# Optimization experiments

Hardware: AMD Instinct MI355X
Metric: run time of the kernel (lower is better)

Reference implementation:

```python
import jax, jax.numpy as jnp
import numpy as np

NEG = -10000.0

def setup_inputs() -> dict:
    key = jax.random.key(0)
    ks = jax.random.split(key, 8)
    B, S, D = 16, 1024, 768
    scale = 1.0 / np.sqrt(D)
    return {
        "q": jax.random.normal(ks[0], (B, S, D), jnp.float32),
        "k": jax.random.normal(ks[1], (B, S, D), jnp.float32),
        "v": jax.random.normal(ks[2], (B, S, D), jnp.float32),
        "Wq": jax.random.normal(ks[3], (D, D), jnp.float32) * scale,
        "bq": jnp.zeros((D,), jnp.float32),
        "Wk": jax.random.normal(ks[4], (D, D), jnp.float32) * scale,
        "bk": jnp.zeros((D,), jnp.float32),
        "Wv": jax.random.normal(ks[5], (D, D), jnp.float32) * scale,
        "bv": jnp.zeros((D,), jnp.float32),
        "temperature": jnp.float32(1.0),
    }

def reference(q, k, v, Wq, bq, Wk, bk, Wv, bv, temperature):
    # Linear projections (torch Linear: x @ W.T + b; here W stored as [out,in])
    Q = jnp.einsum("bsd,ed->bse", q, Wq) + bq  # [B,S,Dq]
    K = jnp.einsum("bsd,ed->bse", k, Wk) + bk  # [B,S,Dk]
    V = jnp.einsum("bsd,ed->bse", v, Wv) + bv  # [B,S,Dv]
    scores = jnp.einsum("bqe,bke->bqk", Q, K) / temperature  # [B,S,S]
    S = scores.shape[-1]
    diag = jnp.eye(S, dtype=bool)  # diagonal self-exclusion mask
    scores = jnp.where(diag[None, :, :], NEG, scores)
    attn = jax.nn.softmax(scores, axis=-1)
    return jnp.einsum("bqk,bke->bqe", attn, V)
```

## Files before the change

kernel.cpp:

```cpp
#include <hip/hip_runtime.h>
#include <math.h>


typedef _Float16 f16x8 __attribute__((ext_vector_type(8)));
typedef _Float16 f16x4 __attribute__((ext_vector_type(4)));
typedef __attribute__((ext_vector_type(4))) float f32x4;

template<typename T>
__device__ __forceinline__ void async_copy16(T* lds, const T* g) {
    __builtin_amdgcn_global_load_lds(
        (const __attribute__((address_space(1))) unsigned int*)g,
        (__attribute__((address_space(3))) unsigned int*)lds, 16, 0, 0);
}

__device__ __forceinline__ void barrier_mem() {
    asm volatile("s_barrier" ::: "memory");
}

template<int EPI, int BIAS>
__global__ __launch_bounds__(512, 2)
void mfma_gemm256(const _Float16* __restrict__ A, const _Float16* __restrict__ B,
                  const float* __restrict__ bias, void* __restrict__ C0,
                  int K, int lda, int ldb, int ldc,
                  long long sA, long long sB, long long sC)
{
    __shared__ _Float16 smem[65536];

    const int tid = threadIdx.x;

    const int gx = gridDim.x, gy = gridDim.y;
    const int nwg = gx * gy * gridDim.z;
    const int p = blockIdx.x + gx * (blockIdx.y + gy * blockIdx.z);
    const int cpx = nwg >> 3;
    const int l = (nwg & 7) ? p : (p & 7) * cpx + (p >> 3);
    const int bx = l % gx;
    const int by = (l / gx) % gy;
    const long long bz = l / (gx * gy);
    const int m0 = by * 256, n0 = bx * 256;

    const _Float16* A0 = A + bz * sA;
    const _Float16* B0 = B + bz * sB;

    const int lane = tid & 63;
    const int wid  = tid >> 6;
    const int wm   = wid >> 2;
    const int wn   = wid & 3;
    const int fr   = lane & 15;
    const int fs   = lane >> 4;

    const int nt = K / 64;
    const int iters = nt / 2;

    auto stage_unit = [&](int dbuf, int isB, int unit, int tile) {
        if (tile >= nt) return;
        const int kt = tile * 64;
        const int lr = tid >> 3, s = tid & 7;
        const int grow = isB ? (unit * 64 + lr)
                             : (((lr >> 5) << 7) + unit * 32 + (lr & 31));
        const int gslot = s ^ (grow & 7);
        _Float16* dst = smem + dbuf * 32768 + isB * 16384 + grow * 64 + s * 8;
        const _Float16* src = (isB ? B0 : A0)
            + (size_t)((isB ? n0 : m0) + grow) * (size_t)(isB ? ldb : lda)
            + kt + gslot * 8;
        async_copy16(dst, src);
    };

    f32x4 acc[8][4] = {};
    f16x8 bf[4][2];

#define PHASE(BUF, Q, READB, STAGES, VMW) do {                                 \
    const _Float16* Ab = smem + (BUF) * 32768;                                 \
    const _Float16* Bb = Ab + 16384;                                           \
    f16x8 a0k0, a0k1, a1k0, a1k1;                                              \
    { const int r = wm * 128 + ((Q) * 2 + 0) * 16 + fr;                        \
      a0k0 = *(const f16x8*)&Ab[r * 64 + ((fs       ^ (r & 7)) * 8)];          \
      a0k1 = *(const f16x8*)&Ab[r * 64 + (((4 + fs) ^ (r & 7)) * 8)]; }        \
    { const int r = wm * 128 + ((Q) * 2 + 1) * 16 + fr;                        \
      a1k0 = *(const f16x8*)&Ab[r * 64 + ((fs       ^ (r & 7)) * 8)];          \
      a1k1 = *(const f16x8*)&Ab[r * 64 + (((4 + fs) ^ (r & 7)) * 8)]; }        \
    if (READB) {                                                               \
      _Pragma("unroll") for (int ni = 0; ni < 4; ++ni) {                       \
        const int r = wn * 64 + ni * 16 + fr;                                  \
        bf[ni][0] = *(const f16x8*)&Bb[r * 64 + ((fs       ^ (r & 7)) * 8)];   \
        bf[ni][1] = *(const f16x8*)&Bb[r * 64 + (((4 + fs) ^ (r & 7)) * 8)]; } \
    }                                                                          \
    STAGES;                                                                    \
    barrier_mem();                                                             \
    __builtin_amdgcn_s_setprio(1);                                             \
    _Pragma("unroll") for (int ni = 0; ni < 4; ++ni) {                         \
      acc[(Q)*2+0][ni] = __builtin_amdgcn_mfma_f32_16x16x32_f16(a0k0, bf[ni][0], acc[(Q)*2+0][ni], 0, 0, 0); \
      acc[(Q)*2+0][ni] = __builtin_amdgcn_mfma_f32_16x16x32_f16(a0k1, bf[ni][1], acc[(Q)*2+0][ni], 0, 0, 0); \
      acc[(Q)*2+1][ni] = __builtin_amdgcn_mfma_f32_16x16x32_f16(a1k0, bf[ni][0], acc[(Q)*2+1][ni], 0, 0, 0); \
      acc[(Q)*2+1][ni] = __builtin_amdgcn_mfma_f32_16x16x32_f16(a1k1, bf[ni][1], acc[(Q)*2+1][ni], 0, 0, 0); \
    }                                                                          \
    __builtin_amdgcn_s_setprio(0);                                             \
    VMW;                                                                       \
    barrier_mem();                                                             \
} while (0)

    stage_unit(0, 0, 0, 0); stage_unit(0, 0, 1, 0);
    stage_unit(0, 0, 2, 0); stage_unit(0, 0, 3, 0);
    stage_unit(0, 1, 0, 0); stage_unit(0, 1, 1, 0);
    stage_unit(0, 1, 2, 0); stage_unit(0, 1, 3, 0);
    stage_unit(1, 1, 0, 1); stage_unit(1, 1, 1, 1);
    stage_unit(1, 1, 2, 1); stage_unit(1, 1, 3, 1);
    stage_unit(1, 0, 0, 1); stage_unit(1, 0, 1, 1);
    asm volatile("s_waitcnt vmcnt(6)" ::: "memory");
    barrier_mem();

    for (int i = 0; i < iters; ++i) {
        const int T1 = 2 * i + 1, T2 = 2 * i + 2, T3 = 2 * i + 3;
        const bool last = (i + 1 == iters);
        PHASE(0, 0, 1, stage_unit(1, 0, 2, T1); stage_unit(1, 0, 3, T1), );
        PHASE(0, 1, 0, stage_unit(0, 1, 0, T2); stage_unit(0, 1, 1, T2), );
        PHASE(0, 2, 0, stage_unit(0, 1, 2, T2); stage_unit(0, 1, 3, T2), );
        PHASE(0, 3, 0, stage_unit(0, 0, 0, T2); stage_unit(0, 0, 1, T2),
              if (last) { asm volatile("s_waitcnt vmcnt(0)" ::: "memory"); }
              else      { asm volatile("s_waitcnt vmcnt(6)" ::: "memory"); });
        PHASE(1, 0, 1, stage_unit(0, 0, 2, T2); stage_unit(0, 0, 3, T2), );
        PHASE(1, 1, 0, stage_unit(1, 1, 0, T3); stage_unit(1, 1, 1, T3), );
        PHASE(1, 2, 0, stage_unit(1, 1, 2, T3); stage_unit(1, 1, 3, T3), );
        PHASE(1, 3, 0, stage_unit(1, 0, 0, T3); stage_unit(1, 0, 1, T3),
              asm volatile("s_waitcnt vmcnt(6)" ::: "memory"));
    }
#undef PHASE

    #pragma unroll
    for (int mi = 0; mi < 8; ++mi) {
        #pragma unroll
        for (int ni = 0; ni < 4; ++ni) {
            const int col = n0 + wn * 64 + ni * 16 + fr;
            #pragma unroll
            for (int r = 0; r < 4; ++r) {
                const int row = m0 + wm * 128 + mi * 16 + fs * 4 + r;
                float vv = acc[mi][ni][r];
                if (BIAS == 1) vv += bias[col];
                if (BIAS == 2) vv += bias[row];
                const size_t idx = (size_t)bz * sC + (size_t)row * ldc + col;
                if (EPI == 0) ((float*)C0)[idx] = vv;
                else          ((_Float16*)C0)[idx] = (_Float16)vv;
            }
        }
    }
}

template<int EPI, int BIAS>
__global__ __launch_bounds__(256, 2)
void mfma_gemm(const _Float16* __restrict__ A, const _Float16* __restrict__ B,
               const float* __restrict__ bias,
               void* __restrict__ C0,
               int K, int lda, int ldb, int ldc,
               long long sA, long long sB, long long sC)
{
    __shared__ _Float16 sAh[128 * 32];
    __shared__ _Float16 sBh[128 * 32];

    const int tid = threadIdx.x;
    const int gx = gridDim.x, gy = gridDim.y;
    const int nwg = gx * gy * gridDim.z;
    const int p = blockIdx.x + gx * (blockIdx.y + gy * blockIdx.z);
    const int cpx = nwg >> 3;
    const int l = (nwg & 7) ? p : (p & 7) * cpx + (p >> 3);
    const int bx = l % gx;
    const int by = (l / gx) % gy;
    const long long bz = l / (gx * gy);

    const int m0 = by * 128;
    const int n0 = bx * 128;

    const _Float16* A0 = A + bz * sA;
    const _Float16* B0 = B + bz * sB;

    const int lrow  = tid >> 2;
    const int lslot = tid & 3;

    const int lane = tid & 63;
    const int wv   = tid >> 6;
    const int wm   = wv >> 1, wn = wv & 1;
    const int fr   = lane & 15;
    const int fs   = lane >> 4;
    const int sw   = fs ^ (fr & 3);
    const int abase = (wm * 64 + fr) * 32 + sw * 8;
    const int bbase = (wn * 64 + fr) * 32 + sw * 8;

    f32x4 acc[4][4] = {};

    for (int kt = 0; kt < K; kt += 32) {
        #pragma unroll
        for (int it = 0; it < 2; ++it) {
            const int row = lrow + it * 64;
            const int gsl = (lslot ^ (row & 3)) << 3;
            const size_t loff = (size_t)tid * 8 + (size_t)it * 2048;
            async_copy16(&sAh[loff], A0 + (size_t)(m0 + row) * lda + kt + gsl);
            async_copy16(&sBh[loff], B0 + (size_t)(n0 + row) * ldb + kt + gsl);
        }
        __syncthreads();

        f16x8 ah[4], bh[4];
        #pragma unroll
        for (int i = 0; i < 4; ++i) {
            ah[i] = *(const f16x8*)&sAh[abase + i * 512];
            bh[i] = *(const f16x8*)&sBh[bbase + i * 512];
        }
        #pragma unroll
        for (int mi = 0; mi < 4; ++mi)
            #pragma unroll
            for (int ni = 0; ni < 4; ++ni)
                acc[mi][ni] = __builtin_amdgcn_mfma_f32_16x16x32_f16(
                    ah[mi], bh[ni], acc[mi][ni], 0, 0, 0);
        __syncthreads();
    }

    const int er = fs * 4;
    #pragma unroll
    for (int mi = 0; mi < 4; ++mi) {
        #pragma unroll
        for (int ni = 0; ni < 4; ++ni) {
            const int col = n0 + wn * 64 + ni * 16 + fr;
            #pragma unroll
            for (int r = 0; r < 4; ++r) {
                const int row = m0 + wm * 64 + mi * 16 + er + r;
                float vv = acc[mi][ni][r];
                if (BIAS == 1) vv += bias[col];
                if (BIAS == 2) vv += bias[row];
                const size_t idx = (size_t)bz * sC + (size_t)row * ldc + col;
                if (EPI == 0) ((float*)C0)[idx] = vv;
                else          ((_Float16*)C0)[idx] = (_Float16)vv;
            }
        }
    }
}

__global__ __launch_bounds__(256)
void tof16_3(const float* __restrict__ q, const float* __restrict__ k,
             const float* __restrict__ v,
             _Float16* __restrict__ qh, _Float16* __restrict__ kh,
             _Float16* __restrict__ vh)
{
    const float* src = blockIdx.z == 0 ? q : blockIdx.z == 1 ? k : v;
    _Float16* dst    = blockIdx.z == 0 ? qh : blockIdx.z == 1 ? kh : vh;
    const long long i = ((long long)blockIdx.x * 256 + threadIdx.x) * 16;
    const float4 a = *(const float4*)&src[i];
    const float4 b = *(const float4*)&src[i + 4];
    const float4 c = *(const float4*)&src[i + 8];
    const float4 d = *(const float4*)&src[i + 12];
    f16x8 o0, o1;
    o0[0] = (_Float16)a.x; o0[1] = (_Float16)a.y;
    o0[2] = (_Float16)a.z; o0[3] = (_Float16)a.w;
    o0[4] = (_Float16)b.x; o0[5] = (_Float16)b.y;
    o0[6] = (_Float16)b.z; o0[7] = (_Float16)b.w;
    o1[0] = (_Float16)c.x; o1[1] = (_Float16)c.y;
    o1[2] = (_Float16)c.z; o1[3] = (_Float16)c.w;
    o1[4] = (_Float16)d.x; o1[5] = (_Float16)d.y;
    o1[6] = (_Float16)d.z; o1[7] = (_Float16)d.w;
    *(f16x8*)&dst[i] = o0;
    *(f16x8*)&dst[i + 8] = o1;
}

__global__ __launch_bounds__(256)
void tof16_kernel(const float* __restrict__ src, _Float16* __restrict__ dst,
                  long long n)
{
    long long i = ((long long)blockIdx.x * 256 + threadIdx.x) * 8;
    const long long stride = (long long)gridDim.x * 2048;
    for (; i < n; i += stride) {
        const float4 a = *(const float4*)&src[i];
        const float4 b = *(const float4*)&src[i + 4];
        f16x8 o;
        o[0] = (_Float16)a.x; o[1] = (_Float16)a.y;
        o[2] = (_Float16)a.z; o[3] = (_Float16)a.w;
        o[4] = (_Float16)b.x; o[5] = (_Float16)b.y;
        o[6] = (_Float16)b.z; o[7] = (_Float16)b.w;
        *(f16x8*)&dst[i] = o;
    }
}

__global__ __launch_bounds__(256)
void transpose_f16(const float* __restrict__ src, _Float16* __restrict__ dst, int n)
{
    __shared__ float t[64][65];
    const int tx = threadIdx.x & 63, ty = threadIdx.x >> 6;
    const int r0 = blockIdx.y * 64, c0 = blockIdx.x * 64;
    #pragma unroll
    for (int r = 0; r < 16; ++r) {
        const int row = ty * 16 + r;
        t[row][tx] = src[(size_t)(r0 + row) * n + c0 + tx];
    }
    __syncthreads();
    #pragma unroll
    for (int r = 0; r < 16; ++r) {
        const int orow = ty * 16 + r;
        dst[(size_t)(c0 + orow) * n + r0 + tx] = (_Float16)t[tx][orow];
    }
}

__global__ __launch_bounds__(256)
void colvec_kernel(const _Float16* __restrict__ WkT, const float* __restrict__ bq,
                   float* __restrict__ colvec, int n)
{
    const int wv = threadIdx.x >> 6, lane = threadIdx.x & 63;
    const int d = blockIdx.x * 4 + wv;
    float s = 0.f;
    for (int e = lane; e < n; e += 64)
        s += (float)WkT[(size_t)d * n + e] * bq[e];
    #pragma unroll
    for (int off = 32; off; off >>= 1) s += __shfl_down(s, off, 64);
    if (lane == 0) colvec[d] = s;
}

__global__ __launch_bounds__(256)
void cterm_kernel(const float* __restrict__ k, const float* __restrict__ colvec,
                  float* __restrict__ cterm)
{
    const int wv = threadIdx.x >> 6, lane = threadIdx.x & 63;
    const long long row = (long long)blockIdx.x * 4 + wv;
    const float* kp = k + row * 768;
    float s = 0.f;
    #pragma unroll
    for (int i = 0; i < 3; ++i) {
        const float4 a = *(const float4*)&kp[lane * 4 + i * 256];
        const float4 c = *(const float4*)&colvec[lane * 4 + i * 256];
        s += a.x * c.x + a.y * c.y + a.z * c.z + a.w * c.w;
    }
    #pragma unroll
    for (int off = 32; off; off >>= 1) s += __shfl_down(s, off, 64);
    if (lane == 0) cterm[row] = s;
}

__global__ __launch_bounds__(256)
void softmax_diag(const float* __restrict__ P, _Float16* __restrict__ Pout,
                  const float* __restrict__ tptr,
                  const float* __restrict__ cterm, int S)
{
    const int p = blockIdx.x;
    const int row = (p & 7) * (16 * 1024 / 8) + (p >> 3);
    const int i   = row % S;
    const float* rp = P + (long long)row * S;
    const int tid = threadIdx.x;
    const float invt = 1.0f / tptr[0];

    const float4 v  = *(const float4*)&rp[tid * 4];
    const float4 ct = *(const float4*)&cterm[(long long)(row / S) * S + tid * 4];
    float vals[4] = {v.x + ct.x, v.y + ct.y, v.z + ct.z, v.w + ct.w};
    #pragma unroll
    for (int j = 0; j < 4; ++j) {
        vals[j] *= invt;
        if (tid * 4 + j == i) vals[j] = -INFINITY;
    }

    float mx = fmaxf(fmaxf(vals[0], vals[1]), fmaxf(vals[2], vals[3]));
    #pragma unroll
    for (int off = 32; off > 0; off >>= 1)
        mx = fmaxf(mx, __shfl_down(mx, off, 64));

    __shared__ float smax[4], ssum[4];
    const int wv = tid >> 6, ln = tid & 63;
    if (ln == 0) smax[wv] = mx;
    __syncthreads();
    mx = fmaxf(fmaxf(smax[0], smax[1]), fmaxf(smax[2], smax[3]));

    float e[4];
    float s = 0.f;
    #pragma unroll
    for (int j = 0; j < 4; ++j) { e[j] = expf(vals[j] - mx); s += e[j]; }
    #pragma unroll
    for (int off = 32; off > 0; off >>= 1)
        s += __shfl_down(s, off, 64);
    if (ln == 0) ssum[wv] = s;
    __syncthreads();
    s = ssum[0] + ssum[1] + ssum[2] + ssum[3];

    const float inv = 1.0f / s;
    f16x4 o;
    o[0] = (_Float16)(e[0] * inv);
    o[1] = (_Float16)(e[1] * inv);
    o[2] = (_Float16)(e[2] * inv);
    o[3] = (_Float16)(e[3] * inv);
    *(f16x4*)&Pout[(long long)row * S + tid * 4] = o;
}

extern "C" void kernel_launch(void* const* d_in, const int* in_sizes, int n_in,
                              void* d_out, int out_size, void* d_ws, size_t ws_size,
                              hipStream_t stream)
{
    const float* q    = (const float*)d_in[0];
    const float* k    = (const float*)d_in[1];
    const float* v    = (const float*)d_in[2];
    const float* Wq   = (const float*)d_in[3];
    const float* bq   = (const float*)d_in[4];
    const float* Wk   = (const float*)d_in[5];
    const float* bk   = (const float*)d_in[6];
    const float* Wv   = (const float*)d_in[7];
    const float* bv   = (const float*)d_in[8];
    const float* temp = (const float*)d_in[9];
    (void)bk;

    const int S = 1024, D = 768;
    const long long nW = (long long)D * D;

    char* ws = (char*)d_ws;
    _Float16* qh  = (_Float16*)(ws + 0);
    _Float16* kh  = (_Float16*)(ws + 25165824);
    _Float16* Pc  = (_Float16*)(ws + 0);
    _Float16* vh  = (_Float16*)(ws + 50331648);
    _Float16* VT  = (_Float16*)(ws + 75497472);
    _Float16* KG  = (_Float16*)(ws + 100663296);
    float*  scores = (float*)(ws + 125829120);
    _Float16* wvh = (_Float16*)(ws + 192937984);
    _Float16* WqT = (_Float16*)(ws + 194117632);
    _Float16* WkT = (_Float16*)(ws + 195297280);
    _Float16* G   = (_Float16*)(ws + 196476928);
    float* colvec = (float*)(ws + 197656576);
    float* cterm  = (float*)(ws + 197659648);

    dim3 blk(256);
    dim3 blk512(512);

    tof16_3<<<dim3(3072, 1, 3), blk, 0, stream>>>(q, k, v, qh, kh, vh);
    tof16_kernel<<<288, blk, 0, stream>>>(Wv, wvh, nW);
    transpose_f16<<<dim3(12, 12), blk, 0, stream>>>(Wq, WqT, D);
    transpose_f16<<<dim3(12, 12), blk, 0, stream>>>(Wk, WkT, D);

    colvec_kernel<<<192,  blk, 0, stream>>>(WkT, bq, colvec, D);
    cterm_kernel <<<4096, blk, 0, stream>>>(k, colvec, cterm);

    mfma_gemm256<1, 2><<<dim3(4, 3, 16), blk512, 0, stream>>>(
        wvh, vh, bv, VT,
        768, 768, 768, 1024, 0, (long long)S * D, (long long)D * S);

    mfma_gemm<1, 0><<<dim3(6, 6, 1), blk, 0, stream>>>(
        WqT, WkT, nullptr, G,
        768, 768, 768, 768, 0, 0, 0);

    mfma_gemm256<1, 0><<<dim3(3, 64, 1), blk512, 0, stream>>>(
        kh, G, nullptr, KG,
        768, 768, 768, 768, 0, 0, 0);

    mfma_gemm256<0, 0><<<dim3(4, 4, 16), blk512, 0, stream>>>(
        qh, KG, nullptr, scores,
        768, 768, 768, 1024,
        (long long)S * D, (long long)S * D, (long long)S * S);

    softmax_diag<<<16 * S, blk, 0, stream>>>(scores, Pc, temp, cterm, S);

    mfma_gemm256<0, 0><<<dim3(3, 4, 16), blk512, 0, stream>>>(
        Pc, VT, nullptr, d_out,
        1024, 1024, 1024, 768,
        (long long)S * S, (long long)D * S, (long long)S * D);
}
```

Baseline: 228.0 us.

## Fuse prep kernels, fold k conversion into cterm, merge KG and VT GEMMs

Replaces the separate q/k/v conversion, Wv conversion and two weight-transpose launches with one block-indexed prep kernel. The k-to-fp16 conversion moves into the cterm kernel, which already reads k, so that tensor is read only once. The K·G and V projection GEMMs, each 192 tiles, become one 384-block launch that interleaves tasks by block index. This is meant to cut launch overhead and underfilled GEMM tails at the cost of runtime-selected parameters in the shared GEMM body.

```diff
diff --git a/kernel.cpp b/kernel.cpp
--- a/kernel.cpp
+++ b/kernel.cpp
@@ -17,30 +17,13 @@
     asm volatile("s_barrier" ::: "memory");
 }
 
-template<int EPI, int BIAS>
-__global__ __launch_bounds__(512, 2)
-void mfma_gemm256(const _Float16* __restrict__ A, const _Float16* __restrict__ B,
-                  const float* __restrict__ bias, void* __restrict__ C0,
-                  int K, int lda, int ldb, int ldc,
-                  long long sA, long long sB, long long sC)
-{
-    __shared__ _Float16 smem[65536];
-
-    const int tid = threadIdx.x;
-
-    const int gx = gridDim.x, gy = gridDim.y;
-    const int nwg = gx * gy * gridDim.z;
-    const int p = blockIdx.x + gx * (blockIdx.y + gy * blockIdx.z);
-    const int cpx = nwg >> 3;
-    const int l = (nwg & 7) ? p : (p & 7) * cpx + (p >> 3);
-    const int bx = l % gx;
-    const int by = (l / gx) % gy;
-    const long long bz = l / (gx * gy);
-    const int m0 = by * 256, n0 = bx * 256;
-
-    const _Float16* A0 = A + bz * sA;
-    const _Float16* B0 = B + bz * sB;
-
+template<int EPI>
+__device__ __forceinline__ void gemm256_body(
+    const _Float16* __restrict__ A0, const _Float16* __restrict__ B0,
+    const float* __restrict__ bias, void* __restrict__ C0,
+    int K, int lda, int ldb, int ldc, long long cbase,
+    int m0, int n0, int bias_mode, int tid, _Float16* smem)
+{
     const int lane = tid & 63;
     const int wid  = tid >> 6;
     const int wm   = wid >> 2;
@@ -134,14 +117,65 @@
             for (int r = 0; r < 4; ++r) {
                 const int row = m0 + wm * 128 + mi * 16 + fs * 4 + r;
                 float vv = acc[mi][ni][r];
-                if (BIAS == 1) vv += bias[col];
-                if (BIAS == 2) vv += bias[row];
-                const size_t idx = (size_t)bz * sC + (size_t)row * ldc + col;
+                if (bias_mode == 1) vv += bias[col];
+                if (bias_mode == 2) vv += bias[row];
+                const size_t idx = (size_t)cbase + (size_t)row * ldc + col;
                 if (EPI == 0) ((float*)C0)[idx] = vv;
                 else          ((_Float16*)C0)[idx] = (_Float16)vv;
             }
         }
     }
+}
+
+template<int EPI, int BIAS>
+__global__ __launch_bounds__(512, 2)
+void mfma_gemm256(const _Float16* __restrict__ A, const _Float16* __restrict__ B,
+                  const float* __restrict__ bias, void* __restrict__ C0,
+                  int K, int lda, int ldb, int ldc,
+                  long long sA, long long sB, long long sC)
+{
+    __shared__ _Float16 smem[65536];
+    const int tid = threadIdx.x;
+    const int gx = gridDim.x, gy = gridDim.y;
+    const int nwg = gx * gy * gridDim.z;
+    const int p = blockIdx.x + gx * (blockIdx.y + gy * blockIdx.z);
+    const int cpx = nwg >> 3;
+    const int l = (nwg & 7) ? p : (p & 7) * cpx + (p >> 3);
+    const int bx = l % gx;
+    const int by = (l / gx) % gy;
+    const long long bz = l / (gx * gy);
+    gemm256_body<EPI>(A + bz * sA, B + bz * sB, bias, C0,
+                      K, lda, ldb, ldc, bz * sC,
+                      by * 256, bx * 256, BIAS, tid, smem);
+}
+
+__global__ __launch_bounds__(512, 2)
+void mfma_gemm256_dual(
+    const _Float16* A_0, const _Float16* B_0, const float* bias_0, void* C_0,
+    int lda_0, int ldb_0, int ldc_0, long long sA_0, long long sB_0,
+    long long sC_0, int gx_0, int gy_0, int bm_0,
+    const _Float16* A_1, const _Float16* B_1, const float* bias_1, void* C_1,
+    int lda_1, int ldb_1, int ldc_1, long long sA_1, long long sB_1,
+    long long sC_1, int gx_1, int gy_1, int bm_1, int K)
+{
+    __shared__ _Float16 smem[65536];
+    const int tid = threadIdx.x;
+    const int p = blockIdx.x;
+    const int task = p & 1;
+    const int l = ((p & 7) >> 1) * 48 + (p >> 3);
+
+    const int gx = task ? gx_1 : gx_0;
+    const int gy = task ? gy_1 : gy_0;
+    const int bx = l % gx;
+    const int by = (l / gx) % gy;
+    const long long bz = l / (gx * gy);
+
+    const _Float16* A = (task ? A_1 : A_0) + bz * (task ? sA_1 : sA_0);
+    const _Float16* B = (task ? B_1 : B_0) + bz * (task ? sB_1 : sB_0);
+    gemm256_body<1>(A, B, task ? bias_1 : bias_0, task ? C_1 : C_0,
+                    K, task ? lda_1 : lda_0, task ? ldb_1 : ldb_0,
+                    task ? ldc_1 : ldc_0, bz * (task ? sC_1 : sC_0),
+                    by * 256, bx * 256, task ? bm_1 : bm_0, tid, smem);
 }
 
 template<int EPI, int BIAS>
@@ -232,65 +266,65 @@
 }
 
 __global__ __launch_bounds__(256)
-void tof16_3(const float* __restrict__ q, const float* __restrict__ k,
-             const float* __restrict__ v,
-             _Float16* __restrict__ qh, _Float16* __restrict__ kh,
-             _Float16* __restrict__ vh)
-{
-    const float* src = blockIdx.z == 0 ? q : blockIdx.z == 1 ? k : v;
-    _Float16* dst    = blockIdx.z == 0 ? qh : blockIdx.z == 1 ? kh : vh;
-    const long long i = ((long long)blockIdx.x * 256 + threadIdx.x) * 16;
-    const float4 a = *(const float4*)&src[i];
-    const float4 b = *(const float4*)&src[i + 4];
-    const float4 c = *(const float4*)&src[i + 8];
-    const float4 d = *(const float4*)&src[i + 12];
-    f16x8 o0, o1;
-    o0[0] = (_Float16)a.x; o0[1] = (_Float16)a.y;
-    o0[2] = (_Float16)a.z; o0[3] = (_Float16)a.w;
-    o0[4] = (_Float16)b.x; o0[5] = (_Float16)b.y;
-    o0[6] = (_Float16)b.z; o0[7] = (_Float16)b.w;
-    o1[0] = (_Float16)c.x; o1[1] = (_Float16)c.y;
-    o1[2] = (_Float16)c.z; o1[3] = (_Float16)c.w;
-    o1[4] = (_Float16)d.x; o1[5] = (_Float16)d.y;
-    o1[6] = (_Float16)d.z; o1[7] = (_Float16)d.w;
-    *(f16x8*)&dst[i] = o0;
-    *(f16x8*)&dst[i + 8] = o1;
-}
-
-__global__ __launch_bounds__(256)
-void tof16_kernel(const float* __restrict__ src, _Float16* __restrict__ dst,
-                  long long n)
-{
-    long long i = ((long long)blockIdx.x * 256 + threadIdx.x) * 8;
-    const long long stride = (long long)gridDim.x * 2048;
-    for (; i < n; i += stride) {
+void fat_prep(const float* __restrict__ q, const float* __restrict__ v,
+              const float* __restrict__ Wq, const float* __restrict__ Wk,
+              const float* __restrict__ Wv,
+              _Float16* __restrict__ qh, _Float16* __restrict__ vh,
+              _Float16* __restrict__ WqT, _Float16* __restrict__ WkT,
+              _Float16* __restrict__ wvh)
+{
+    __shared__ float t[64][65];
+    const int p = blockIdx.x;
+    const int tid = threadIdx.x;
+
+    if (p < 6144) {
+        const float* src = p < 3072 ? q : v;
+        _Float16* dst    = p < 3072 ? qh : vh;
+        const long long i = ((long long)(p < 3072 ? p : p - 3072) * 256 + tid) * 16;
         const float4 a = *(const float4*)&src[i];
         const float4 b = *(const float4*)&src[i + 4];
+        const float4 c = *(const float4*)&src[i + 8];
+        const float4 d = *(const float4*)&src[i + 12];
+        f16x8 o0, o1;
+        o0[0] = (_Float16)a.x; o0[1] = (_Float16)a.y;
+        o0[2] = (_Float16)a.z; o0[3] = (_Float16)a.w;
+        o0[4] = (_Float16)b.x; o0[5] = (_Float16)b.y;
+        o0[6] = (_Float16)b.z; o0[7] = (_Float16)b.w;
+        o1[0] = (_Float16)c.x; o1[1] = (_Float16)c.y;
+        o1[2] = (_Float16)c.z; o1[3] = (_Float16)c.w;
+        o1[4] = (_Float16)d.x; o1[5] = (_Float16)d.y;
+        o1[6] = (_Float16)d.z; o1[7] = (_Float16)d.w;
+        *(f16x8*)&dst[i] = o0;
+        *(f16x8*)&dst[i + 8] = o1;
+        return;
+    }
+    if (p < 6432) {
+        const long long i = ((long long)(p - 6144) * 256 + tid) * 8;
+        const float4 a = *(const float4*)&Wv[i];
+        const float4 b = *(const float4*)&Wv[i + 4];
         f16x8 o;
         o[0] = (_Float16)a.x; o[1] = (_Float16)a.y;
         o[2] = (_Float16)a.z; o[3] = (_Float16)a.w;
         o[4] = (_Float16)b.x; o[5] = (_Float16)b.y;
         o[6] = (_Float16)b.z; o[7] = (_Float16)b.w;
-        *(f16x8*)&dst[i] = o;
-    }
-}
-
-__global__ __launch_bounds__(256)
-void transpose_f16(const float* __restrict__ src, _Float16* __restrict__ dst, int n)
-{
-    __shared__ float t[64][65];
-    const int tx = threadIdx.x & 63, ty = threadIdx.x >> 6;
-    const int r0 = blockIdx.y * 64, c0 = blockIdx.x * 64;
+        *(f16x8*)&wvh[i] = o;
+        return;
+    }
+    const int tno = p < 6576 ? p - 6432 : p - 6576;
+    const float* src = p < 6576 ? Wq : Wk;
+    _Float16* dst    = p < 6576 ? WqT : WkT;
+    const int r0 = (tno / 12) * 64, c0 = (tno % 12) * 64;
+    const int tx = tid & 63, ty = tid >> 6;
     #pragma unroll
     for (int r = 0; r < 16; ++r) {
         const int row = ty * 16 + r;
-        t[row][tx] = src[(size_t)(r0 + row) * n + c0 + tx];
+        t[row][tx] = src[(size_t)(r0 + row) * 768 + c0 + tx];
     }
     __syncthreads();
     #pragma unroll
     for (int r = 0; r < 16; ++r) {
         const int orow = ty * 16 + r;
-        dst[(size_t)(c0 + orow) * n + r0 + tx] = (_Float16)t[tx][orow];
+        dst[(size_t)(c0 + orow) * 768 + r0 + tx] = (_Float16)t[tx][orow];
     }
 }
 
@@ -309,18 +343,23 @@
 }
 
 __global__ __launch_bounds__(256)
-void cterm_kernel(const float* __restrict__ k, const float* __restrict__ colvec,
-                  float* __restrict__ cterm)
+void cterm_cvt_kernel(const float* __restrict__ k, const float* __restrict__ colvec,
+                      float* __restrict__ cterm, _Float16* __restrict__ kh)
 {
     const int wv = threadIdx.x >> 6, lane = threadIdx.x & 63;
     const long long row = (long long)blockIdx.x * 4 + wv;
     const float* kp = k + row * 768;
+    _Float16* op = kh + row * 768;
     float s = 0.f;
     #pragma unroll
     for (int i = 0; i < 3; ++i) {
         const float4 a = *(const float4*)&kp[lane * 4 + i * 256];
         const float4 c = *(const float4*)&colvec[lane * 4 + i * 256];
         s += a.x * c.x + a.y * c.y + a.z * c.z + a.w * c.w;
+        f16x4 o;
+        o[0] = (_Float16)a.x; o[1] = (_Float16)a.y;
+        o[2] = (_Float16)a.z; o[3] = (_Float16)a.w;
+        *(f16x4*)&op[lane * 4 + i * 256] = o;
     }
     #pragma unroll
     for (int off = 32; off; off >>= 1) s += __shfl_down(s, off, 64);
@@ -396,7 +435,6 @@
     (void)bk;
 
     const int S = 1024, D = 768;
-    const long long nW = (long long)D * D;
 
     char* ws = (char*)d_ws;
     _Float16* qh  = (_Float16*)(ws + 0);
@@ -416,25 +454,19 @@
     dim3 blk(256);
     dim3 blk512(512);
 
-    tof16_3<<<dim3(3072, 1, 3), blk, 0, stream>>>(q, k, v, qh, kh, vh);
-    tof16_kernel<<<288, blk, 0, stream>>>(Wv, wvh, nW);
-    transpose_f16<<<dim3(12, 12), blk, 0, stream>>>(Wq, WqT, D);
-    transpose_f16<<<dim3(12, 12), blk, 0, stream>>>(Wk, WkT, D);
-
-    colvec_kernel<<<192,  blk, 0, stream>>>(WkT, bq, colvec, D);
-    cterm_kernel <<<4096, blk, 0, stream>>>(k, colvec, cterm);
-
-    mfma_gemm256<1, 2><<<dim3(4, 3, 16), blk512, 0, stream>>>(
-        wvh, vh, bv, VT,
-        768, 768, 768, 1024, 0, (long long)S * D, (long long)D * S);
+    fat_prep<<<6720, blk, 0, stream>>>(q, v, Wq, Wk, Wv, qh, vh, WqT, WkT, wvh);
+
+    colvec_kernel<<<192, blk, 0, stream>>>(WkT, bq, colvec, D);
+    cterm_cvt_kernel<<<4096, blk, 0, stream>>>(k, colvec, cterm, kh);
 
     mfma_gemm<1, 0><<<dim3(6, 6, 1), blk, 0, stream>>>(
         WqT, WkT, nullptr, G,
         768, 768, 768, 768, 0, 0, 0);
 
-    mfma_gemm256<1, 0><<<dim3(3, 64, 1), blk512, 0, stream>>>(
-        kh, G, nullptr, KG,
-        768, 768, 768, 768, 0, 0, 0);
+    mfma_gemm256_dual<<<384, blk512, 0, stream>>>(
+        kh, G, nullptr, KG, 768, 768, 768, 0, 0, 0, 3, 64, 0,
+        wvh, vh, bv, VT, 768, 768, 1024, 0, (long long)S * D, (long long)D * S,
+        4, 3, 2, 768);
 
     mfma_gemm256<0, 0><<<dim3(4, 4, 16), blk512, 0, stream>>>(
         qh, KG, nullptr, scores,
```

Measured after the change: 237.5 us. +4.2%, slower.
